# Kernel optimization log

Hardware: AMD Instinct MI355X
Metric: run time of the kernel (lower is better)

The kernel has to match this reference:

```python
import jax, jax.numpy as jnp
import numpy as np

T, C, H = 4096, 1024, 16
D = C // H  # head dim = 64


def setup_inputs() -> dict:
    key = jax.random.key(0)
    k1, k2, k3 = jax.random.split(key, 3)
    x = jax.random.normal(k1, (T, C), dtype=jnp.float32)
    w_attn = jax.random.normal(k2, (C, 3 * C), dtype=jnp.float32) * (1.0 / np.sqrt(C))
    w_proj = jax.random.normal(k3, (C, C), dtype=jnp.float32) * (1.0 / np.sqrt(C))
    return {"x": x, "w_attn": w_attn, "w_proj": w_proj, "num_frames": 64}


def reference(x, w_attn, w_proj, num_frames):
    t, c = x.shape
    d = c // H
    qkv = x @ w_attn                       # (T, 3C)
    q, k, v = jnp.split(qkv, 3, axis=-1)   # each (T, C)
    # (T, H, D) -> (H, T, D)
    q = q.reshape(t, H, d).transpose(1, 0, 2)
    k = k.reshape(t, H, d).transpose(1, 0, 2)
    v = v.reshape(t, H, d).transpose(1, 0, 2)
    # causal mask with dense global prefix: every query may attend to the
    # first num_frames keys in addition to the causal lower triangle.
    rows = jnp.arange(t)[:, None]
    cols = jnp.arange(t)[None, :]
    mask = (cols <= rows) | (cols < num_frames)   # (T, T) bool
    scores = jnp.einsum('htd,hsd->hts', q, k) * (1.0 / np.sqrt(d))  # (H,T,T)
    scores = jnp.where(mask[None], scores, jnp.float32(-jnp.inf))
    att = jax.nn.softmax(scores, axis=-1)
    y = jnp.einsum('hts,hsd->htd', att, v)        # (H, T, D)
    y = y.transpose(1, 0, 2).reshape(t, c)        # (T, C)
    return y @ w_proj
```

## Files before the change

### kernel.cpp

```cpp
#include <hip/hip_runtime.h>
#include <hip/hip_bf16.h>

#define Tq 4096
#define Cdim 1024
#define NH 16
#define DH 64

typedef __attribute__((ext_vector_type(8))) short short8;
typedef __attribute__((ext_vector_type(4))) float f32x4;

__device__ __forceinline__ unsigned short f2bf(float f) {
  union { float f; unsigned int u; } v; v.f = f;
  unsigned int r = v.u + 0x7FFFu + ((v.u >> 16) & 1u);
  return (unsigned short)(r >> 16);
}

__device__ __forceinline__ unsigned int cvtpk_bf16(float lo, float hi) {
  unsigned int r;
  asm volatile("v_cvt_pk_bf16_f32 %0, %1, %2" : "=v"(r) : "v"(lo), "v"(hi));
  return r;
}

__global__ void cvt_kernel(const float* __restrict__ in, unsigned short* __restrict__ out, int n) {
  int idx = (blockIdx.x * blockDim.x + threadIdx.x) * 4;
  if (idx + 3 < n) {
    float4 v = *reinterpret_cast<const float4*>(in + idx);
    ushort4 o;
    o.x = f2bf(v.x); o.y = f2bf(v.y); o.z = f2bf(v.z); o.w = f2bf(v.w);
    *reinterpret_cast<ushort4*>(out + idx) = o;
  }
}

__global__ void transpose_cvt(const float* __restrict__ in, unsigned short* __restrict__ out,
                              int R, int Ccols) {
  __shared__ float tile[64][65];
  int c0 = blockIdx.x * 64, r0 = blockIdx.y * 64;
  int tx = threadIdx.x & 63;
  int ty = threadIdx.x >> 6;
  #pragma unroll
  for (int rr = 0; rr < 64; rr += 4)
    tile[rr + ty][tx] = in[(r0 + rr + ty) * Ccols + c0 + tx];
  __syncthreads();
  #pragma unroll
  for (int rr = 0; rr < 64; rr += 4)
    out[(c0 + rr + ty) * R + r0 + tx] = f2bf(tile[tx][rr + ty]);
}

template<int OUT_MODE>
__global__ __launch_bounds__(256, 3)
void gemm_bt(const unsigned short* __restrict__ A,
             const unsigned short* __restrict__ B,
             void* __restrict__ Cout,
             int M, int N, int K)
{
  __shared__ __align__(16) unsigned short As[128][64];
  __shared__ __align__(16) unsigned short Bs[128][64];
  const int tid = threadIdx.x;
  const int lane = tid & 63;
  const int wave = tid >> 6;
  const int wm = wave >> 1, wn = wave & 1;
  const int m0 = blockIdx.y * 128, n0 = blockIdx.x * 128;

  f32x4 acc[4][4] = {};

  const int lrow = lane >> 3;
  const int lcol = (lane & 7) * 8;

  for (int k0 = 0; k0 < K; k0 += 64) {
    __syncthreads();
    #pragma unroll
    for (int t = 0; t < 4; ++t) {
      const int r = wave * 32 + t * 8;
      __builtin_amdgcn_global_load_lds(
        (const __attribute__((address_space(1))) void*)&A[(size_t)(m0 + r + lrow) * K + k0 + lcol],
        (__attribute__((address_space(3))) void*)&As[r][0], 16, 0, 0);
      __builtin_amdgcn_global_load_lds(
        (const __attribute__((address_space(1))) void*)&B[(size_t)(n0 + r + lrow) * K + k0 + lcol],
        (__attribute__((address_space(3))) void*)&Bs[r][0], 16, 0, 0);
    }
    __syncthreads();
    #pragma unroll
    for (int kk = 0; kk < 64; kk += 32) {
      const int frow = lane & 15;
      const int fcol = kk + 8 * (lane >> 4);
      short8 a[4], b[4];
      #pragma unroll
      for (int i = 0; i < 4; ++i) {
        a[i] = *reinterpret_cast<const short8*>(&As[wm * 64 + i * 16 + frow][fcol]);
        b[i] = *reinterpret_cast<const short8*>(&Bs[wn * 64 + i * 16 + frow][fcol]);
      }
      #pragma unroll
      for (int i = 0; i < 4; ++i)
        #pragma unroll
        for (int j = 0; j < 4; ++j)
          acc[i][j] = __builtin_amdgcn_mfma_f32_16x16x32_bf16(a[i], b[j], acc[i][j], 0, 0, 0);
    }
  }

  const int rbase = (lane >> 4) * 4;
  const int ccol = lane & 15;
  #pragma unroll
  for (int i = 0; i < 4; ++i) {
    const int row0 = m0 + wm * 64 + i * 16 + rbase;
    #pragma unroll
    for (int j = 0; j < 4; ++j) {
      const int col = n0 + wn * 64 + j * 16 + ccol;
      if (OUT_MODE == 0) {
        unsigned short* q = (unsigned short*)Cout;
        int sec = col >> 10, rem = col & 1023;
        int hh = rem >> 6, d = rem & 63;
        if (sec == 2) {
          ushort4 pk;
          pk.x = f2bf(acc[i][j][0]); pk.y = f2bf(acc[i][j][1]);
          pk.z = f2bf(acc[i][j][2]); pk.w = f2bf(acc[i][j][3]);
          *reinterpret_cast<ushort4*>(
              &q[((size_t)(2 * NH + hh) * DH + d) * Tq + row0]) = pk;
        } else {
          #pragma unroll
          for (int r = 0; r < 4; ++r)
            q[(((size_t)sec * NH + hh) * Tq + row0 + r) * DH + d] = f2bf(acc[i][j][r]);
        }
      } else {
        #pragma unroll
        for (int r = 0; r < 4; ++r)
          ((float*)Cout)[(row0 + r) * N + col] = acc[i][j][r];
      }
    }
  }
}

__global__ __launch_bounds__(512, 4)
void attn_kernel(const unsigned short* __restrict__ qkv,
                 unsigned short* __restrict__ y,
                 const int* __restrict__ nf_ptr)
{
  __shared__ __align__(16) unsigned short Ks[2][64][72];
  __shared__ __align__(16) unsigned short VTs[2][64][72];

  const int tid  = threadIdx.x;
  const int lane = tid & 63;
  const int w    = tid >> 6;
  const int g    = lane >> 4;
  const int li   = lane & 15;

  const int h  = blockIdx.x & 15;
  const int iq = (blockIdx.x >> 4) & 15;
  const int hi = blockIdx.x >> 8;
  const int qc = hi ? iq : 31 - iq;
  const int q0 = qc * 128;
  const int nf = nf_ptr[0];

  const unsigned short* Qh  = qkv + (size_t)h * Tq * DH;
  const unsigned short* Kh  = qkv + (size_t)(NH + h) * Tq * DH;
  const unsigned short* VTh = qkv + (size_t)(2 * NH + h) * DH * Tq;

  const int qrow = q0 + w * 16 + li;
  short8 qf[2];
  #pragma unroll
  for (int kk = 0; kk < 2; ++kk)
    qf[kk] = *reinterpret_cast<const short8*>(&Qh[qrow * DH + kk * 32 + 8 * g]);

  f32x4 o[4] = {};
  f32x4 ol = {};
  float m_r = -1e30f;

  short8 ones;
  #pragma unroll
  for (int e = 0; e < 8; ++e) ones[e] = (short)0x3F80;

  int lastt = q0 + 127;
  if (nf - 1 > lastt) lastt = nf - 1;
  const int ktend = lastt >> 6;

  const float SCL = 0.125f * 1.44269504f;

  const int srow = tid >> 3;
  const int scol = (tid & 7) * 8;

  *reinterpret_cast<short8*>(&Ks[0][srow][scol]) =
      *reinterpret_cast<const short8*>(&Kh[srow * DH + scol]);
  *reinterpret_cast<short8*>(&VTs[0][srow][scol]) =
      *reinterpret_cast<const short8*>(&VTh[(size_t)srow * Tq + scol]);
  __syncthreads();

  int cur = 0;
  for (int kt = 0; kt <= ktend; ++kt) {
    const int kv0 = kt * 64;
    const bool havenext = (kt < ktend);
    short8 nk, nv;
    if (havenext) {
      nk = *reinterpret_cast<const short8*>(&Kh[(kv0 + 64 + srow) * DH + scol]);
      nv = *reinterpret_cast<const short8*>(&VTh[(size_t)srow * Tq + kv0 + 64 + scol]);
    }

    f32x4 s[4];
    #pragma unroll
    for (int nb = 0; nb < 4; ++nb) {
      f32x4 a = {};
      #pragma unroll
      for (int kk = 0; kk < 2; ++kk) {
        short8 kf = *reinterpret_cast<const short8*>(
            &Ks[cur][nb * 16 + li][kk * 32 + 8 * g]);
        a = __builtin_amdgcn_mfma_f32_16x16x32_bf16(kf, qf[kk], a, 0, 0, 0);
      }
      s[nb] = a;
    }

    const bool needmask = !((kv0 + 63 <= q0 + w * 16) || (kv0 + 63 < nf));
    float p[4][4];
    #pragma unroll
    for (int nb = 0; nb < 4; ++nb) {
      #pragma unroll
      for (int r = 0; r < 4; ++r) {
        float v = s[nb][r] * SCL;
        if (needmask) {
          const int kvi = kv0 + nb * 16 + 4 * g + r;
          if (!(kvi <= qrow || kvi < nf)) v = -1e30f;
        }
        p[nb][r] = v;
      }
    }

    float mx = p[0][0];
    #pragma unroll
    for (int nb = 0; nb < 4; ++nb)
      #pragma unroll
      for (int r = 0; r < 4; ++r)
        mx = fmaxf(mx, p[nb][r]);
    mx = fmaxf(mx, __shfl_xor(mx, 16, 64));
    mx = fmaxf(mx, __shfl_xor(mx, 32, 64));

    if (!__all(mx <= m_r + 8.0f)) {
      float newm = fmaxf(m_r, mx);
      float alpha = exp2f(m_r - newm);
      m_r = newm;
      #pragma unroll
      for (int db = 0; db < 4; ++db)
        #pragma unroll
        for (int r = 0; r < 4; ++r)
          o[db][r] *= alpha;
      ol[0] *= alpha;
    }

    #pragma unroll
    for (int nb = 0; nb < 4; ++nb)
      #pragma unroll
      for (int r = 0; r < 4; ++r)
        p[nb][r] = exp2f(p[nb][r] - m_r);

    #pragma unroll
    for (int kk = 0; kk < 2; ++kk) {
      unsigned int X1 = cvtpk_bf16(p[2 * kk][0], p[2 * kk][1]);
      unsigned int X2 = cvtpk_bf16(p[2 * kk][2], p[2 * kk][3]);
      unsigned int Y1 = cvtpk_bf16(p[2 * kk + 1][0], p[2 * kk + 1][1]);
      unsigned int Y2 = cvtpk_bf16(p[2 * kk + 1][2], p[2 * kk + 1][3]);
      asm volatile("v_permlane32_swap_b32 %0, %1" : "+v"(X1), "+v"(Y1));
      asm volatile("v_permlane32_swap_b32 %0, %1" : "+v"(X2), "+v"(Y2));
      asm volatile("v_permlane16_swap_b32 %0, %1" : "+v"(X1), "+v"(Y1));
      asm volatile("v_permlane16_swap_b32 %0, %1" : "+v"(X2), "+v"(Y2));
      union { unsigned int u[4]; short8 s8; } W;
      W.u[0] = X1; W.u[1] = X2; W.u[2] = Y1; W.u[3] = Y2;
      #pragma unroll
      for (int db = 0; db < 4; ++db) {
        short8 vb = *reinterpret_cast<const short8*>(
            &VTs[cur][db * 16 + li][kk * 32 + 8 * g]);
        o[db] = __builtin_amdgcn_mfma_f32_16x16x32_bf16(vb, W.s8, o[db], 0, 0, 0);
      }
      ol = __builtin_amdgcn_mfma_f32_16x16x32_bf16(ones, W.s8, ol, 0, 0, 0);
    }

    if (havenext) {
      *reinterpret_cast<short8*>(&Ks[cur ^ 1][srow][scol]) = nk;
      *reinterpret_cast<short8*>(&VTs[cur ^ 1][srow][scol]) = nv;
    }
    __syncthreads();
    cur ^= 1;
  }

  const float inv = 1.0f / ol[0];
  unsigned short* yp = y + (size_t)qrow * Cdim + h * DH;
  #pragma unroll
  for (int db = 0; db < 4; ++db) {
    ushort4 pk;
    pk.x = f2bf(o[db][0] * inv);
    pk.y = f2bf(o[db][1] * inv);
    pk.z = f2bf(o[db][2] * inv);
    pk.w = f2bf(o[db][3] * inv);
    *reinterpret_cast<ushort4*>(&yp[db * 16 + 4 * g]) = pk;
  }
}

extern "C" void kernel_launch(void* const* d_in, const int* in_sizes, int n_in,
                              void* d_out, int out_size, void* d_ws, size_t ws_size,
                              hipStream_t stream) {
  (void)in_sizes; (void)n_in; (void)out_size; (void)ws_size;
  const float* x  = (const float*)d_in[0];
  const float* wa = (const float*)d_in[1];
  const float* wp = (const float*)d_in[2];
  const int*   nf = (const int*)d_in[3];
  float* out = (float*)d_out;

  char* ws = (char*)d_ws;
  unsigned short* x_bf = (unsigned short*)(ws);
  unsigned short* waT  = (unsigned short*)(ws + (size_t)8  * 1024 * 1024);
  unsigned short* wpT  = (unsigned short*)(ws + (size_t)14 * 1024 * 1024);
  unsigned short* qkvb = (unsigned short*)(ws + (size_t)16 * 1024 * 1024);
  unsigned short* ybf  = (unsigned short*)(ws + (size_t)40 * 1024 * 1024);

  cvt_kernel<<<4096, 256, 0, stream>>>(x, x_bf, Tq * Cdim);
  transpose_cvt<<<dim3(48, 16), 256, 0, stream>>>(wa, waT, 1024, 3072);
  transpose_cvt<<<dim3(16, 16), 256, 0, stream>>>(wp, wpT, 1024, 1024);
  gemm_bt<0><<<dim3(24, 32), 256, 0, stream>>>(x_bf, waT, (void*)qkvb, Tq, 3 * Cdim, Cdim);
  attn_kernel<<<512, 512, 0, stream>>>(qkvb, ybf, nf);
  gemm_bt<1><<<dim3(Cdim / 128, Tq / 128), 256, 0, stream>>>(ybf, wpT, (void*)out, Tq, Cdim, Cdim);
}
```

Measured before the change: 165.2 us.

## Give each attention wave two 16-row query tiles to reuse K/V fragments

The attention block shrinks from 8 to 4 waves, and each wave now handles 32 query rows as two 16-row sub-tiles. K fragments are loaded from LDS once per tile and reused for both sub-tiles, and V fragments are shared across both P·V MFMAs. The scale multiply is folded into an fma inside the exp2, and the rescale threshold is expressed in raw score units. This halves LDS fragment reads per query row and block-level syncs per row, at the cost of higher register pressure, fewer waves per block, and twice as many K/V tile loads per thread.

```diff
diff --git a/kernel.cpp b/kernel.cpp
--- a/kernel.cpp
+++ b/kernel.cpp
@@ -129,7 +129,7 @@
   }
 }
 
-__global__ __launch_bounds__(512, 4)
+__global__ __launch_bounds__(256, 3)
 void attn_kernel(const unsigned short* __restrict__ qkv,
                  unsigned short* __restrict__ y,
                  const int* __restrict__ nf_ptr)
@@ -154,15 +154,20 @@
   const unsigned short* Kh  = qkv + (size_t)(NH + h) * Tq * DH;
   const unsigned short* VTh = qkv + (size_t)(2 * NH + h) * DH * Tq;
 
-  const int qrow = q0 + w * 16 + li;
-  short8 qf[2];
-  #pragma unroll
-  for (int kk = 0; kk < 2; ++kk)
-    qf[kk] = *reinterpret_cast<const short8*>(&Qh[qrow * DH + kk * 32 + 8 * g]);
-
-  f32x4 o[4] = {};
-  f32x4 ol = {};
-  float m_r = -1e30f;
+  int qrow[2];
+  qrow[0] = q0 + w * 32 + li;
+  qrow[1] = q0 + w * 32 + 16 + li;
+  short8 qf[2][2];
+  #pragma unroll
+  for (int r0 = 0; r0 < 2; ++r0)
+    #pragma unroll
+    for (int kk = 0; kk < 2; ++kk)
+      qf[r0][kk] = *reinterpret_cast<const short8*>(
+          &Qh[qrow[r0] * DH + kk * 32 + 8 * g]);
+
+  f32x4 o[2][4] = {};
+  f32x4 ol[2] = {};
+  float m_r[2] = {-1e30f, -1e30f};
 
   short8 ones;
   #pragma unroll
@@ -173,120 +178,153 @@
   const int ktend = lastt >> 6;
 
   const float SCL = 0.125f * 1.44269504f;
-
-  const int srow = tid >> 3;
-  const int scol = (tid & 7) * 8;
-
-  *reinterpret_cast<short8*>(&Ks[0][srow][scol]) =
-      *reinterpret_cast<const short8*>(&Kh[srow * DH + scol]);
-  *reinterpret_cast<short8*>(&VTs[0][srow][scol]) =
-      *reinterpret_cast<const short8*>(&VTh[(size_t)srow * Tq + scol]);
+  const float THR_RAW = 8.0f / SCL;
+
+  const int rr = tid >> 3;
+  const int sc = (tid & 7) * 8;
+
+  *reinterpret_cast<short8*>(&Ks[0][rr][sc]) =
+      *reinterpret_cast<const short8*>(&Kh[rr * DH + sc]);
+  *reinterpret_cast<short8*>(&Ks[0][rr + 32][sc]) =
+      *reinterpret_cast<const short8*>(&Kh[(rr + 32) * DH + sc]);
+  *reinterpret_cast<short8*>(&VTs[0][rr][sc]) =
+      *reinterpret_cast<const short8*>(&VTh[(size_t)rr * Tq + sc]);
+  *reinterpret_cast<short8*>(&VTs[0][rr + 32][sc]) =
+      *reinterpret_cast<const short8*>(&VTh[(size_t)(rr + 32) * Tq + sc]);
   __syncthreads();
 
   int cur = 0;
   for (int kt = 0; kt <= ktend; ++kt) {
     const int kv0 = kt * 64;
     const bool havenext = (kt < ktend);
-    short8 nk, nv;
+    short8 nk0, nk1, nv0, nv1;
     if (havenext) {
-      nk = *reinterpret_cast<const short8*>(&Kh[(kv0 + 64 + srow) * DH + scol]);
-      nv = *reinterpret_cast<const short8*>(&VTh[(size_t)srow * Tq + kv0 + 64 + scol]);
-    }
-
-    f32x4 s[4];
-    #pragma unroll
-    for (int nb = 0; nb < 4; ++nb) {
-      f32x4 a = {};
+      const int nx = kv0 + 64;
+      nk0 = *reinterpret_cast<const short8*>(&Kh[(nx + rr) * DH + sc]);
+      nk1 = *reinterpret_cast<const short8*>(&Kh[(nx + rr + 32) * DH + sc]);
+      nv0 = *reinterpret_cast<const short8*>(&VTh[(size_t)rr * Tq + nx + sc]);
+      nv1 = *reinterpret_cast<const short8*>(&VTh[(size_t)(rr + 32) * Tq + nx + sc]);
+    }
+
+    short8 kf[4][2];
+    #pragma unroll
+    for (int nb = 0; nb < 4; ++nb)
+      #pragma unroll
+      for (int kk = 0; kk < 2; ++kk)
+        kf[nb][kk] = *reinterpret_cast<const short8*>(
+            &Ks[cur][nb * 16 + li][kk * 32 + 8 * g]);
+
+    short8 W[2][2];
+
+    #pragma unroll
+    for (int r0 = 0; r0 < 2; ++r0) {
+      f32x4 s[4];
+      #pragma unroll
+      for (int nb = 0; nb < 4; ++nb) {
+        f32x4 a = {};
+        #pragma unroll
+        for (int kk = 0; kk < 2; ++kk)
+          a = __builtin_amdgcn_mfma_f32_16x16x32_bf16(kf[nb][kk], qf[r0][kk], a, 0, 0, 0);
+        s[nb] = a;
+      }
+
+      const bool needmask = !((kv0 + 63 <= q0 + w * 32 + r0 * 16) || (kv0 + 63 < nf));
+      float p[4][4];
+      #pragma unroll
+      for (int nb = 0; nb < 4; ++nb) {
+        #pragma unroll
+        for (int r = 0; r < 4; ++r) {
+          float v = s[nb][r];
+          if (needmask) {
+            const int kvi = kv0 + nb * 16 + 4 * g + r;
+            if (!(kvi <= qrow[r0] || kvi < nf)) v = -1e30f;
+          }
+          p[nb][r] = v;
+        }
+      }
+
+      float mx = p[0][0];
+      #pragma unroll
+      for (int nb = 0; nb < 4; ++nb)
+        #pragma unroll
+        for (int r = 0; r < 4; ++r)
+          mx = fmaxf(mx, p[nb][r]);
+      mx = fmaxf(mx, __shfl_xor(mx, 16, 64));
+      mx = fmaxf(mx, __shfl_xor(mx, 32, 64));
+
+      if (!__all(mx <= m_r[r0] + THR_RAW)) {
+        float newm = fmaxf(m_r[r0], mx);
+        float alpha = exp2f((m_r[r0] - newm) * SCL);
+        m_r[r0] = newm;
+        #pragma unroll
+        for (int db = 0; db < 4; ++db)
+          #pragma unroll
+          for (int r = 0; r < 4; ++r)
+            o[r0][db][r] *= alpha;
+        ol[r0][0] *= alpha;
+      }
+
+      const float mterm = -m_r[r0] * SCL;
+      #pragma unroll
+      for (int nb = 0; nb < 4; ++nb)
+        #pragma unroll
+        for (int r = 0; r < 4; ++r)
+          p[nb][r] = exp2f(__builtin_fmaf(p[nb][r], SCL, mterm));
+
       #pragma unroll
       for (int kk = 0; kk < 2; ++kk) {
-        short8 kf = *reinterpret_cast<const short8*>(
-            &Ks[cur][nb * 16 + li][kk * 32 + 8 * g]);
-        a = __builtin_amdgcn_mfma_f32_16x16x32_bf16(kf, qf[kk], a, 0, 0, 0);
-      }
-      s[nb] = a;
-    }
-
-    const bool needmask = !((kv0 + 63 <= q0 + w * 16) || (kv0 + 63 < nf));
-    float p[4][4];
-    #pragma unroll
-    for (int nb = 0; nb < 4; ++nb) {
-      #pragma unroll
-      for (int r = 0; r < 4; ++r) {
-        float v = s[nb][r] * SCL;
-        if (needmask) {
-          const int kvi = kv0 + nb * 16 + 4 * g + r;
-          if (!(kvi <= qrow || kvi < nf)) v = -1e30f;
-        }
-        p[nb][r] = v;
-      }
-    }
-
-    float mx = p[0][0];
-    #pragma unroll
-    for (int nb = 0; nb < 4; ++nb)
-      #pragma unroll
-      for (int r = 0; r < 4; ++r)
-        mx = fmaxf(mx, p[nb][r]);
-    mx = fmaxf(mx, __shfl_xor(mx, 16, 64));
-    mx = fmaxf(mx, __shfl_xor(mx, 32, 64));
-
-    if (!__all(mx <= m_r + 8.0f)) {
-      float newm = fmaxf(m_r, mx);
-      float alpha = exp2f(m_r - newm);
-      m_r = newm;
-      #pragma unroll
-      for (int db = 0; db < 4; ++db)
-        #pragma unroll
-        for (int r = 0; r < 4; ++r)
-          o[db][r] *= alpha;
-      ol[0] *= alpha;
-    }
-
-    #pragma unroll
-    for (int nb = 0; nb < 4; ++nb)
-      #pragma unroll
-      for (int r = 0; r < 4; ++r)
-        p[nb][r] = exp2f(p[nb][r] - m_r);
+        unsigned int X1 = cvtpk_bf16(p[2 * kk][0], p[2 * kk][1]);
+        unsigned int X2 = cvtpk_bf16(p[2 * kk][2], p[2 * kk][3]);
+        unsigned int Y1 = cvtpk_bf16(p[2 * kk + 1][0], p[2 * kk + 1][1]);
+        unsigned int Y2 = cvtpk_bf16(p[2 * kk + 1][2], p[2 * kk + 1][3]);
+        asm volatile("v_permlane32_swap_b32 %0, %1" : "+v"(X1), "+v"(Y1));
+        asm volatile("v_permlane32_swap_b32 %0, %1" : "+v"(X2), "+v"(Y2));
+        asm volatile("v_permlane16_swap_b32 %0, %1" : "+v"(X1), "+v"(Y1));
+        asm volatile("v_permlane16_swap_b32 %0, %1" : "+v"(X2), "+v"(Y2));
+        union { unsigned int u[4]; short8 s8; } Wt;
+        Wt.u[0] = X1; Wt.u[1] = X2; Wt.u[2] = Y1; Wt.u[3] = Y2;
+        W[r0][kk] = Wt.s8;
+      }
+    }
 
     #pragma unroll
     for (int kk = 0; kk < 2; ++kk) {
-      unsigned int X1 = cvtpk_bf16(p[2 * kk][0], p[2 * kk][1]);
-      unsigned int X2 = cvtpk_bf16(p[2 * kk][2], p[2 * kk][3]);
-      unsigned int Y1 = cvtpk_bf16(p[2 * kk + 1][0], p[2 * kk + 1][1]);
-      unsigned int Y2 = cvtpk_bf16(p[2 * kk + 1][2], p[2 * kk + 1][3]);
-      asm volatile("v_permlane32_swap_b32 %0, %1" : "+v"(X1), "+v"(Y1));
-      asm volatile("v_permlane32_swap_b32 %0, %1" : "+v"(X2), "+v"(Y2));
-      asm volatile("v_permlane16_swap_b32 %0, %1" : "+v"(X1), "+v"(Y1));
-      asm volatile("v_permlane16_swap_b32 %0, %1" : "+v"(X2), "+v"(Y2));
-      union { unsigned int u[4]; short8 s8; } W;
-      W.u[0] = X1; W.u[1] = X2; W.u[2] = Y1; W.u[3] = Y2;
       #pragma unroll
       for (int db = 0; db < 4; ++db) {
         short8 vb = *reinterpret_cast<const short8*>(
             &VTs[cur][db * 16 + li][kk * 32 + 8 * g]);
-        o[db] = __builtin_amdgcn_mfma_f32_16x16x32_bf16(vb, W.s8, o[db], 0, 0, 0);
-      }
-      ol = __builtin_amdgcn_mfma_f32_16x16x32_bf16(ones, W.s8, ol, 0, 0, 0);
+        #pragma unroll
+        for (int r0 = 0; r0 < 2; ++r0)
+          o[r0][db] = __builtin_amdgcn_mfma_f32_16x16x32_bf16(vb, W[r0][kk], o[r0][db], 0, 0, 0);
+      }
+      #pragma unroll
+      for (int r0 = 0; r0 < 2; ++r0)
+        ol[r0] = __builtin_amdgcn_mfma_f32_16x16x32_bf16(ones, W[r0][kk], ol[r0], 0, 0, 0);
     }
 
     if (havenext) {
-      *reinterpret_cast<short8*>(&Ks[cur ^ 1][srow][scol]) = nk;
-      *reinterpret_cast<short8*>(&VTs[cur ^ 1][srow][scol]) = nv;
+      *reinterpret_cast<short8*>(&Ks[cur ^ 1][rr][sc]) = nk0;
+      *reinterpret_cast<short8*>(&Ks[cur ^ 1][rr + 32][sc]) = nk1;
+      *reinterpret_cast<short8*>(&VTs[cur ^ 1][rr][sc]) = nv0;
+      *reinterpret_cast<short8*>(&VTs[cur ^ 1][rr + 32][sc]) = nv1;
     }
     __syncthreads();
     cur ^= 1;
   }
 
-  const float inv = 1.0f / ol[0];
-  unsigned short* yp = y + (size_t)qrow * Cdim + h * DH;
-  #pragma unroll
-  for (int db = 0; db < 4; ++db) {
-    ushort4 pk;
-    pk.x = f2bf(o[db][0] * inv);
-    pk.y = f2bf(o[db][1] * inv);
-    pk.z = f2bf(o[db][2] * inv);
-    pk.w = f2bf(o[db][3] * inv);
-    *reinterpret_cast<ushort4*>(&yp[db * 16 + 4 * g]) = pk;
+  #pragma unroll
+  for (int r0 = 0; r0 < 2; ++r0) {
+    const float inv = 1.0f / ol[r0][0];
+    unsigned short* yp = y + (size_t)qrow[r0] * Cdim + h * DH;
+    #pragma unroll
+    for (int db = 0; db < 4; ++db) {
+      ushort4 pk;
+      pk.x = f2bf(o[r0][db][0] * inv);
+      pk.y = f2bf(o[r0][db][1] * inv);
+      pk.z = f2bf(o[r0][db][2] * inv);
+      pk.w = f2bf(o[r0][db][3] * inv);
+      *reinterpret_cast<ushort4*>(&yp[db * 16 + 4 * g]) = pk;
+    }
   }
 }
 
@@ -311,6 +349,6 @@
   transpose_cvt<<<dim3(48, 16), 256, 0, stream>>>(wa, waT, 1024, 3072);
   transpose_cvt<<<dim3(16, 16), 256, 0, stream>>>(wp, wpT, 1024, 1024);
   gemm_bt<0><<<dim3(24, 32), 256, 0, stream>>>(x_bf, waT, (void*)qkvb, Tq, 3 * Cdim, Cdim);
-  attn_kernel<<<512, 512, 0, stream>>>(qkvb, ybf, nf);
+  attn_kernel<<<512, 256, 0, stream>>>(qkvb, ybf, nf);
   gemm_bt<1><<<dim3(Cdim / 128, Tq / 128), 256, 0, stream>>>(ybf, wpT, (void*)out, Tq, Cdim, Cdim);
 }
```

New measurement: 191.2 us. 1.16x slower.

## Widen attention KV tile to 128 keys and fold scale into exp2 FMA

Applied to the files above, without the earlier changes.

The attention loop now stages 128 keys per iteration (two 64-key halves processed inside) instead of 64, halving the number of __syncthreads barriers and global prefetch rounds per query block. It also defers the softmax scale, comparing raw scores against a rescaled threshold and computing exp2 via a single FMA with the scale and negated max. The trade is roughly double LDS usage per block (which may reduce occupancy under the 4-blocks launch bound), more live prefetch registers, and up to 64 extra masked keys processed at the causal tail.

```diff
diff --git a/kernel.cpp b/kernel.cpp
--- a/kernel.cpp
+++ b/kernel.cpp
@@ -134,8 +134,8 @@
                  unsigned short* __restrict__ y,
                  const int* __restrict__ nf_ptr)
 {
-  __shared__ __align__(16) unsigned short Ks[2][64][72];
-  __shared__ __align__(16) unsigned short VTs[2][64][72];
+  __shared__ __align__(16) unsigned short Ks[2][128][72];
+  __shared__ __align__(16) unsigned short VTs[2][64][136];
 
   const int tid  = threadIdx.x;
   const int lane = tid & 63;
@@ -170,108 +170,126 @@
 
   int lastt = q0 + 127;
   if (nf - 1 > lastt) lastt = nf - 1;
-  const int ktend = lastt >> 6;
+  const int ktend = lastt >> 7;
 
   const float SCL = 0.125f * 1.44269504f;
-
-  const int srow = tid >> 3;
-  const int scol = (tid & 7) * 8;
-
-  *reinterpret_cast<short8*>(&Ks[0][srow][scol]) =
-      *reinterpret_cast<const short8*>(&Kh[srow * DH + scol]);
-  *reinterpret_cast<short8*>(&VTs[0][srow][scol]) =
-      *reinterpret_cast<const short8*>(&VTh[(size_t)srow * Tq + scol]);
+  const float THR_RAW = 8.0f / SCL;
+
+  const int krow0 = tid >> 3;
+  const int kcol  = (tid & 7) * 8;
+  const int vrow0 = tid >> 4;
+  const int vcol  = (tid & 15) * 8;
+
+  *reinterpret_cast<short8*>(&Ks[0][krow0][kcol]) =
+      *reinterpret_cast<const short8*>(&Kh[krow0 * DH + kcol]);
+  *reinterpret_cast<short8*>(&Ks[0][krow0 + 64][kcol]) =
+      *reinterpret_cast<const short8*>(&Kh[(krow0 + 64) * DH + kcol]);
+  *reinterpret_cast<short8*>(&VTs[0][vrow0][vcol]) =
+      *reinterpret_cast<const short8*>(&VTh[(size_t)vrow0 * Tq + vcol]);
+  *reinterpret_cast<short8*>(&VTs[0][vrow0 + 32][vcol]) =
+      *reinterpret_cast<const short8*>(&VTh[(size_t)(vrow0 + 32) * Tq + vcol]);
   __syncthreads();
 
   int cur = 0;
   for (int kt = 0; kt <= ktend; ++kt) {
-    const int kv0 = kt * 64;
+    const int kv0 = kt * 128;
     const bool havenext = (kt < ktend);
-    short8 nk, nv;
+    short8 nk0, nk1, nv0, nv1;
     if (havenext) {
-      nk = *reinterpret_cast<const short8*>(&Kh[(kv0 + 64 + srow) * DH + scol]);
-      nv = *reinterpret_cast<const short8*>(&VTh[(size_t)srow * Tq + kv0 + 64 + scol]);
-    }
-
-    f32x4 s[4];
+      const int nx = kv0 + 128;
+      nk0 = *reinterpret_cast<const short8*>(&Kh[(nx + krow0) * DH + kcol]);
+      nk1 = *reinterpret_cast<const short8*>(&Kh[(nx + krow0 + 64) * DH + kcol]);
+      nv0 = *reinterpret_cast<const short8*>(&VTh[(size_t)vrow0 * Tq + nx + vcol]);
+      nv1 = *reinterpret_cast<const short8*>(&VTh[(size_t)(vrow0 + 32) * Tq + nx + vcol]);
+    }
+
     #pragma unroll
-    for (int nb = 0; nb < 4; ++nb) {
-      f32x4 a = {};
+    for (int h2 = 0; h2 < 2; ++h2) {
+      const int kvb = kv0 + h2 * 64;
+
+      f32x4 s[4];
+      #pragma unroll
+      for (int nb = 0; nb < 4; ++nb) {
+        f32x4 a = {};
+        #pragma unroll
+        for (int kk = 0; kk < 2; ++kk) {
+          short8 kf = *reinterpret_cast<const short8*>(
+              &Ks[cur][h2 * 64 + nb * 16 + li][kk * 32 + 8 * g]);
+          a = __builtin_amdgcn_mfma_f32_16x16x32_bf16(kf, qf[kk], a, 0, 0, 0);
+        }
+        s[nb] = a;
+      }
+
+      const bool needmask = !((kvb + 63 <= q0 + w * 16) || (kvb + 63 < nf));
+      float p[4][4];
+      #pragma unroll
+      for (int nb = 0; nb < 4; ++nb) {
+        #pragma unroll
+        for (int r = 0; r < 4; ++r) {
+          float v = s[nb][r];
+          if (needmask) {
+            const int kvi = kvb + nb * 16 + 4 * g + r;
+            if (!(kvi <= qrow || kvi < nf)) v = -1e30f;
+          }
+          p[nb][r] = v;
+        }
+      }
+
+      float mx = p[0][0];
+      #pragma unroll
+      for (int nb = 0; nb < 4; ++nb)
+        #pragma unroll
+        for (int r = 0; r < 4; ++r)
+          mx = fmaxf(mx, p[nb][r]);
+      mx = fmaxf(mx, __shfl_xor(mx, 16, 64));
+      mx = fmaxf(mx, __shfl_xor(mx, 32, 64));
+
+      if (!__all(mx <= m_r + THR_RAW)) {
+        float newm = fmaxf(m_r, mx);
+        float alpha = exp2f((m_r - newm) * SCL);
+        m_r = newm;
+        #pragma unroll
+        for (int db = 0; db < 4; ++db)
+          #pragma unroll
+          for (int r = 0; r < 4; ++r)
+            o[db][r] *= alpha;
+        ol[0] *= alpha;
+      }
+
+      const float mterm = -m_r * SCL;
+      #pragma unroll
+      for (int nb = 0; nb < 4; ++nb)
+        #pragma unroll
+        for (int r = 0; r < 4; ++r)
+          p[nb][r] = exp2f(__builtin_fmaf(p[nb][r], SCL, mterm));
+
       #pragma unroll
       for (int kk = 0; kk < 2; ++kk) {
-        short8 kf = *reinterpret_cast<const short8*>(
-            &Ks[cur][nb * 16 + li][kk * 32 + 8 * g]);
-        a = __builtin_amdgcn_mfma_f32_16x16x32_bf16(kf, qf[kk], a, 0, 0, 0);
-      }
-      s[nb] = a;
-    }
-
-    const bool needmask = !((kv0 + 63 <= q0 + w * 16) || (kv0 + 63 < nf));
-    float p[4][4];
-    #pragma unroll
-    for (int nb = 0; nb < 4; ++nb) {
-      #pragma unroll
-      for (int r = 0; r < 4; ++r) {
-        float v = s[nb][r] * SCL;
-        if (needmask) {
-          const int kvi = kv0 + nb * 16 + 4 * g + r;
-          if (!(kvi <= qrow || kvi < nf)) v = -1e30f;
+        unsigned int X1 = cvtpk_bf16(p[2 * kk][0], p[2 * kk][1]);
+        unsigned int X2 = cvtpk_bf16(p[2 * kk][2], p[2 * kk][3]);
+        unsigned int Y1 = cvtpk_bf16(p[2 * kk + 1][0], p[2 * kk + 1][1]);
+        unsigned int Y2 = cvtpk_bf16(p[2 * kk + 1][2], p[2 * kk + 1][3]);
+        asm volatile("v_permlane32_swap_b32 %0, %1" : "+v"(X1), "+v"(Y1));
+        asm volatile("v_permlane32_swap_b32 %0, %1" : "+v"(X2), "+v"(Y2));
+        asm volatile("v_permlane16_swap_b32 %0, %1" : "+v"(X1), "+v"(Y1));
+        asm volatile("v_permlane16_swap_b32 %0, %1" : "+v"(X2), "+v"(Y2));
+        union { unsigned int u[4]; short8 s8; } W;
+        W.u[0] = X1; W.u[1] = X2; W.u[2] = Y1; W.u[3] = Y2;
+        #pragma unroll
+        for (int db = 0; db < 4; ++db) {
+          short8 vb = *reinterpret_cast<const short8*>(
+              &VTs[cur][db * 16 + li][h2 * 64 + kk * 32 + 8 * g]);
+          o[db] = __builtin_amdgcn_mfma_f32_16x16x32_bf16(vb, W.s8, o[db], 0, 0, 0);
         }
-        p[nb][r] = v;
-      }
-    }
-
-    float mx = p[0][0];
-    #pragma unroll
-    for (int nb = 0; nb < 4; ++nb)
-      #pragma unroll
-      for (int r = 0; r < 4; ++r)
-        mx = fmaxf(mx, p[nb][r]);
-    mx = fmaxf(mx, __shfl_xor(mx, 16, 64));
-    mx = fmaxf(mx, __shfl_xor(mx, 32, 64));
-
-    if (!__all(mx <= m_r + 8.0f)) {
-      float newm = fmaxf(m_r, mx);
-      float alpha = exp2f(m_r - newm);
-      m_r = newm;
-      #pragma unroll
-      for (int db = 0; db < 4; ++db)
-        #pragma unroll
-        for (int r = 0; r < 4; ++r)
-          o[db][r] *= alpha;
-      ol[0] *= alpha;
-    }
-
-    #pragma unroll
-    for (int nb = 0; nb < 4; ++nb)
-      #pragma unroll
-      for (int r = 0; r < 4; ++r)
-        p[nb][r] = exp2f(p[nb][r] - m_r);
-
-    #pragma unroll
-    for (int kk = 0; kk < 2; ++kk) {
-      unsigned int X1 = cvtpk_bf16(p[2 * kk][0], p[2 * kk][1]);
-      unsigned int X2 = cvtpk_bf16(p[2 * kk][2], p[2 * kk][3]);
-      unsigned int Y1 = cvtpk_bf16(p[2 * kk + 1][0], p[2 * kk + 1][1]);
-      unsigned int Y2 = cvtpk_bf16(p[2 * kk + 1][2], p[2 * kk + 1][3]);
-      asm volatile("v_permlane32_swap_b32 %0, %1" : "+v"(X1), "+v"(Y1));
-      asm volatile("v_permlane32_swap_b32 %0, %1" : "+v"(X2), "+v"(Y2));
-      asm volatile("v_permlane16_swap_b32 %0, %1" : "+v"(X1), "+v"(Y1));
-      asm volatile("v_permlane16_swap_b32 %0, %1" : "+v"(X2), "+v"(Y2));
-      union { unsigned int u[4]; short8 s8; } W;
-      W.u[0] = X1; W.u[1] = X2; W.u[2] = Y1; W.u[3] = Y2;
-      #pragma unroll
-      for (int db = 0; db < 4; ++db) {
-        short8 vb = *reinterpret_cast<const short8*>(
-            &VTs[cur][db * 16 + li][kk * 32 + 8 * g]);
-        o[db] = __builtin_amdgcn_mfma_f32_16x16x32_bf16(vb, W.s8, o[db], 0, 0, 0);
-      }
-      ol = __builtin_amdgcn_mfma_f32_16x16x32_bf16(ones, W.s8, ol, 0, 0, 0);
+        ol = __builtin_amdgcn_mfma_f32_16x16x32_bf16(ones, W.s8, ol, 0, 0, 0);
+      }
     }
 
     if (havenext) {
-      *reinterpret_cast<short8*>(&Ks[cur ^ 1][srow][scol]) = nk;
-      *reinterpret_cast<short8*>(&VTs[cur ^ 1][srow][scol]) = nv;
+      *reinterpret_cast<short8*>(&Ks[cur ^ 1][krow0][kcol]) = nk0;
+      *reinterpret_cast<short8*>(&Ks[cur ^ 1][krow0 + 64][kcol]) = nk1;
+      *reinterpret_cast<short8*>(&VTs[cur ^ 1][vrow0][vcol]) = nv0;
+      *reinterpret_cast<short8*>(&VTs[cur ^ 1][vrow0 + 32][vcol]) = nv1;
     }
     __syncthreads();
     cur ^= 1;
```

Measured after the change: 163.4 us. About the same (-1.1%).
